# Performance work log

Measured on AMD Instinct MI355X. Metric: run time of the kernel, lower is better.

The kernel has to match this reference:

```python
import jax, jax.numpy as jnp
import numpy as np

T, HID, H = 1024, 2048, 16
LQ, LKV = 1536, 512
DR, DN, DQ, DV = 64, 128, 192, 128
HI, DI, TOPK = 16, 128, 256
EPS = 1e-6
NEG = -1e30


def _rms(x, g, eps=EPS):
    return x * jax.lax.rsqrt(jnp.mean(x * x, -1, keepdims=True) + eps) * g


def _ln(x, w, b, eps=1e-6):
    m = jnp.mean(x, -1, keepdims=True)
    v = jnp.mean((x - m) ** 2, -1, keepdims=True)
    return (x - m) * jax.lax.rsqrt(v + eps) * w + b


def _rope_interleave(x, cos, sin):
    # HF apply_rotary_pos_emb_interleave: de-interleave even/odd then standard rotate_half.
    x1, x2 = x[..., 0::2], x[..., 1::2]
    xr = jnp.concatenate([x1, x2], -1)
    rot = jnp.concatenate([-x2, x1], -1)
    return xr * cos + rot * sin


def _sparse_indices(hidden, q_lat, cos, sin, ks, ke, i_wqb, i_wk, i_ln_w, i_ln_b, i_wproj):
    # hidden [T,HID], q_lat [T,LQ]; returns [T,TOPK] int32 (sentinel index = T)
    t = hidden.shape[0]
    q_idx = (q_lat @ i_wqb.T).reshape(t, HI, DI)
    k_idx = _ln(hidden @ i_wk.T, i_ln_w, i_ln_b)          # [T,DI]
    w = hidden @ i_wproj.T                                 # [T,HI]
    q_pe = _rope_interleave(q_idx[..., :DR], cos[:, None, :], sin[:, None, :])
    k_pe = _rope_interleave(k_idx[..., :DR], cos, sin)
    qi = jnp.concatenate([q_pe, q_idx[..., DR:]], -1)      # [T,HI,DI]
    ki = jnp.concatenate([k_pe, k_idx[..., DR:]], -1)      # [T,DI]
    weight_scale = DI ** -0.5 * HI ** -0.5
    logits = jnp.einsum('thd,sd->ths', qi, ki)             # [T,HI,T]
    score = jnp.einsum('ths,th->ts', jax.nn.relu(logits), w) * weight_scale
    pos = jnp.arange(t)
    valid = (pos[None, :] >= ks[:, None]) & (pos[None, :] <= ke[:, None])
    score = jnp.where(valid, score, NEG)
    vals, idx = jax.lax.top_k(score, TOPK)
    return jnp.where(vals <= NEG / 2, t, idx).astype(jnp.int32)


def reference(hidden_states, cos, sin, ks, ke,
              w_qa, g_qa, w_qb, w_kva, g_kva, w_kvb, w_o,
              i_wqb, i_wk, i_ln_w, i_ln_b, i_wproj):
    t = hidden_states.shape[1]
    # low-rank projections
    q_lat = _rms(hidden_states @ w_qa.T, g_qa)             # [1,T,LQ]
    ckv = hidden_states @ w_kva.T                          # [1,T,LKV+DR]
    k_c = _rms(ckv[..., :LKV], g_kva)                      # [1,T,LKV]
    k_r = _rope_interleave(ckv[..., LKV:], cos[None], sin[None])  # [1,T,DR]
    # fp8 indexer (reference math in fp32), no-grad in original
    indices = _sparse_indices(hidden_states[0], q_lat[0], cos, sin, ks, ke,
                              i_wqb, i_wk, i_ln_w, i_ln_b, i_wproj)  # [T,TOPK]
    # MLA up-proj with weight absorption
    q_full = (q_lat @ w_qb.T).reshape(1, t, H, DQ)
    q_nope, q_rope = q_full[..., :DN], q_full[..., DN:]
    q_rope = _rope_interleave(q_rope, cos[None, :, None, :], sin[None, :, None, :])
    w_b = w_kvb.reshape(H, DN + DV, LKV)
    w_kn, w_v = w_b[:, :DN, :], w_b[:, DN:, :]
    q_abs = jnp.einsum('bshd,hdk->bshk', q_nope, w_kn)     # absorb k_nope up-proj
    sq = jnp.concatenate([q_abs, q_rope], -1)[0]           # [T,H,LKV+DR]
    skv = jnp.concatenate([k_c, k_r], -1)[0]               # [T,LKV+DR]
    skv = jnp.concatenate([skv, jnp.zeros((1, LKV + DR), skv.dtype)], 0)  # sentinel row
    # sparse attention over gathered top-k KV rows
    kv_g = skv[indices]                                    # [T,TOPK,LKV+DR]
    logits = jnp.einsum('thd,tjd->thj', sq, kv_g) * (DQ ** -0.5)
    logits = jnp.where(indices[:, None, :] == t, NEG, logits)
    p = jax.nn.softmax(logits, -1)
    out = jnp.einsum('thj,tjk->thk', p, kv_g[..., :LKV])   # values = compressed kv
    o = jnp.einsum('thk,hdk->thd', out, w_v)               # un-absorb v up-proj
    return o.reshape(1, t, H * DV) @ w_o.T


def setup_inputs() -> dict:
    key = jax.random.key(0)
    k = jax.random.split(key, 12)
    n = lambda kk, shape, s: jax.random.normal(kk, shape, jnp.float32) * s
    pos = jnp.arange(T, dtype=jnp.float32)
    inv = 1.0 / (10000.0 ** (jnp.arange(0, DR, 2, dtype=jnp.float32) / DR))
    ang = pos[:, None] * inv[None, :]
    cos = jnp.concatenate([jnp.cos(ang), jnp.cos(ang)], -1)
    sin = jnp.concatenate([jnp.sin(ang), jnp.sin(ang)], -1)
    return dict(
        hidden_states=n(k[0], (1, T, HID), 1.0),
        cos=cos, sin=sin,
        ks=jnp.zeros((T,), jnp.int32),
        ke=jnp.arange(T, dtype=jnp.int32),  # causal: keys s <= t valid
        w_qa=n(k[1], (LQ, HID), HID ** -0.5),
        g_qa=jnp.ones((LQ,), jnp.float32),
        w_qb=n(k[2], (H * DQ, LQ), LQ ** -0.5),
        w_kva=n(k[3], (LKV + DR, HID), HID ** -0.5),
        g_kva=jnp.ones((LKV,), jnp.float32),
        w_kvb=n(k[4], (H * (DN + DV), LKV), LKV ** -0.5),
        w_o=n(k[5], (HID, H * DV), (H * DV) ** -0.5),
        i_wqb=n(k[6], (HI * DI, LQ), LQ ** -0.5),
        i_wk=n(k[7], (DI, HID), HID ** -0.5),
        i_ln_w=jnp.ones((DI,), jnp.float32),
        i_ln_b=jnp.zeros((DI,), jnp.float32),
        i_wproj=n(k[8], (HI, HID), HID ** -0.5),
    )
```

## Files before the change

### kernel.cpp

```cpp
#include <hip/hip_runtime.h>
#include <hip/hip_bf16.h>
#include <cmath>

#define T_ 1024
#define HID_ 2048
#define H_ 16
#define LQ_ 1536
#define LKV_ 512
#define DR_ 64
#define DN_ 128
#define DQ_ 192
#define DV_ 128
#define HI_ 16
#define DI_ 128
#define TOPK_ 256
#define NEGF (-1e30f)

typedef short bfrag_t __attribute__((ext_vector_type(8)));
typedef float f32x4 __attribute__((ext_vector_type(4)));

__device__ __forceinline__ float wave_sum64(float v) {
#pragma unroll
  for (int off = 32; off; off >>= 1) v += __shfl_xor(v, off);
  return v;
}

#define GLL(g, l) __builtin_amdgcn_global_load_lds((const __attribute__((address_space(1))) void*)(g), \
                                     (__attribute__((address_space(3))) void*)(l), 16, 0, 0)

__global__ __launch_bounds__(256) void zero_k(float4* __restrict__ p, int n4) {
  int i = blockIdx.x * 256 + threadIdx.x;
  if (i < n4) p[i] = make_float4(0.f, 0.f, 0.f, 0.f);
}

template<typename CT>
__global__ __launch_bounds__(256) void gemm_bf_k(
    const short* __restrict__ A, int lda, long long sA,
    const short* __restrict__ B, int ldb, long long sB,
    CT* __restrict__ C, int ldc, long long sC,
    int Nout, int K)
{
  __shared__ short As[2][128 * 32];
  __shared__ short Bs[2][128 * 32];
  A += (long long)blockIdx.z * sA;
  B += (long long)blockIdx.z * sB;
  C += (long long)blockIdx.z * sC;
  const int tid = threadIdx.x;
  const int bm = blockIdx.y * 128, bn = blockIdx.x * 128;
  const int wave = tid >> 6, lane = tid & 63;
  const int wm = (wave >> 1) * 64, wn = (wave & 1) * 64;
  const int sr = tid >> 2;
  const int scol = (tid & 3) * 8;
  const int m0 = lane & 15, koff = (lane >> 4) * 8;
  f32x4 acc[4][4] = {};
  const short* ga = A + (long long)(bm + sr) * lda + scol;
  const short* gb = B + (long long)(bn + sr) * ldb + scol;
#define STAGE_BF(buf, off) \
    GLL(ga + (off), As[buf] + tid * 8); GLL(ga + (off) + 64 * lda, As[buf] + tid * 8 + 2048); \
    GLL(gb + (off), Bs[buf] + tid * 8); GLL(gb + (off) + 64 * ldb, Bs[buf] + tid * 8 + 2048);
  const int niter = K >> 5;
  STAGE_BF(0, 0);
  for (int it = 0; it < niter; ++it) {
    const int cur = it & 1;
    if (it + 1 < niter) {
      STAGE_BF(cur ^ 1, (it + 1) * 32);
      asm volatile("s_waitcnt vmcnt(4)\ns_barrier" ::: "memory");
    } else {
      asm volatile("s_waitcnt vmcnt(0)\ns_barrier" ::: "memory");
    }
    bfrag_t af[4], bfv[4];
#pragma unroll
    for (int i = 0; i < 4; ++i)
      af[i] = *(const bfrag_t*)(As[cur] + (wm + i * 16 + m0) * 32 + koff);
#pragma unroll
    for (int j = 0; j < 4; ++j)
      bfv[j] = *(const bfrag_t*)(Bs[cur] + (wn + j * 16 + m0) * 32 + koff);
#pragma unroll
    for (int i = 0; i < 4; ++i)
#pragma unroll
      for (int j = 0; j < 4; ++j)
        acc[i][j] = __builtin_amdgcn_mfma_f32_16x16x32_bf16(af[i], bfv[j], acc[i][j], 0, 0, 0);
    asm volatile("s_barrier" ::: "memory");
  }
#undef STAGE_BF
  const int cr = (lane >> 4) * 4, cc = lane & 15;
#pragma unroll
  for (int i = 0; i < 4; ++i) {
    int row = bm + wm + i * 16 + cr;
#pragma unroll
    for (int j = 0; j < 4; ++j) {
      int col = bn + wn + j * 16 + cc;
      if (col < Nout) {
#pragma unroll
        for (int r = 0; r < 4; ++r)
          C[(long long)(row + r) * ldc + col] = (CT)(acc[i][j][r]);
      }
    }
  }
}

__global__ __launch_bounds__(256) void gemm_bfs_k(
    const short* __restrict__ A, int lda,
    const short* __restrict__ B, int ldb,
    float* __restrict__ C, int ldc, int Nout, int K)
{
  __shared__ short As[2][128 * 32];
  __shared__ short Bs[2][128 * 32];
  const long long kbase = (long long)blockIdx.z * K;
  const int tid = threadIdx.x;
  const int bm = blockIdx.y * 128, bn = blockIdx.x * 128;
  const int wave = tid >> 6, lane = tid & 63;
  const int wm = (wave >> 1) * 64, wn = (wave & 1) * 64;
  const int sr = tid >> 2;
  const int scol = (tid & 3) * 8;
  const int m0 = lane & 15, koff = (lane >> 4) * 8;
  f32x4 acc[4][4] = {};
  const short* ga = A + (long long)(bm + sr) * lda + kbase + scol;
  const short* gb = B + (long long)(bn + sr) * ldb + kbase + scol;
#define STAGE_BS(buf, off) \
    GLL(ga + (off), As[buf] + tid * 8); GLL(ga + (off) + 64 * lda, As[buf] + tid * 8 + 2048); \
    GLL(gb + (off), Bs[buf] + tid * 8); GLL(gb + (off) + 64 * ldb, Bs[buf] + tid * 8 + 2048);
  const int niter = K >> 5;
  STAGE_BS(0, 0);
  for (int it = 0; it < niter; ++it) {
    const int cur = it & 1;
    if (it + 1 < niter) {
      STAGE_BS(cur ^ 1, (it + 1) * 32);
      asm volatile("s_waitcnt vmcnt(4)\ns_barrier" ::: "memory");
    } else {
      asm volatile("s_waitcnt vmcnt(0)\ns_barrier" ::: "memory");
    }
    bfrag_t af[4], bfv[4];
#pragma unroll
    for (int i = 0; i < 4; ++i)
      af[i] = *(const bfrag_t*)(As[cur] + (wm + i * 16 + m0) * 32 + koff);
#pragma unroll
    for (int j = 0; j < 4; ++j)
      bfv[j] = *(const bfrag_t*)(Bs[cur] + (wn + j * 16 + m0) * 32 + koff);
#pragma unroll
    for (int i = 0; i < 4; ++i)
#pragma unroll
      for (int j = 0; j < 4; ++j)
        acc[i][j] = __builtin_amdgcn_mfma_f32_16x16x32_bf16(af[i], bfv[j], acc[i][j], 0, 0, 0);
    asm volatile("s_barrier" ::: "memory");
  }
#undef STAGE_BS
  const int cr = (lane >> 4) * 4, cc = lane & 15;
#pragma unroll
  for (int i = 0; i < 4; ++i) {
    int row = bm + wm + i * 16 + cr;
#pragma unroll
    for (int j = 0; j < 4; ++j) {
      int col = bn + wn + j * 16 + cc;
      if (col < Nout) {
#pragma unroll
        for (int r = 0; r < 4; ++r)
          atomicAdd(&C[(long long)(row + r) * ldc + col], acc[i][j][r]);
      }
    }
  }
}

__global__ __launch_bounds__(256) void gemm3_k(
    const short* __restrict__ Ah, const short* __restrict__ Al, int lda,
    const short* __restrict__ Bh, const short* __restrict__ Bl, int ldb,
    float* __restrict__ C, int ldc, int Nout, int K)
{
  __shared__ short Ahs[2][128 * 32];
  __shared__ short Als[2][128 * 32];
  __shared__ short Bhs[2][128 * 32];
  __shared__ short Bls[2][128 * 32];
  const long long kbase = (long long)blockIdx.z * K;
  const int tid = threadIdx.x;
  const int bm = blockIdx.y * 128, bn = blockIdx.x * 128;
  const int wave = tid >> 6, lane = tid & 63;
  const int wm = (wave >> 1) * 64, wn = (wave & 1) * 64;
  const int sr = tid >> 2;
  const int scol = (tid & 3) * 8;
  const int m0 = lane & 15, koff = (lane >> 4) * 8;
  f32x4 acc[4][4] = {};
  const short* gah = Ah + (long long)(bm + sr) * lda + kbase + scol;
  const short* gal = Al + (long long)(bm + sr) * lda + kbase + scol;
  const short* gbh = Bh + (long long)(bn + sr) * ldb + kbase + scol;
  const short* gbl = Bl + (long long)(bn + sr) * ldb + kbase + scol;
#define STAGE_3(buf, off) \
    GLL(gah + (off), Ahs[buf] + tid * 8); GLL(gah + (off) + 64 * lda, Ahs[buf] + tid * 8 + 2048); \
    GLL(gal + (off), Als[buf] + tid * 8); GLL(gal + (off) + 64 * lda, Als[buf] + tid * 8 + 2048); \
    GLL(gbh + (off), Bhs[buf] + tid * 8); GLL(gbh + (off) + 64 * ldb, Bhs[buf] + tid * 8 + 2048); \
    GLL(gbl + (off), Bls[buf] + tid * 8); GLL(gbl + (off) + 64 * ldb, Bls[buf] + tid * 8 + 2048);
  const int niter = K >> 5;
  STAGE_3(0, 0);
  for (int it = 0; it < niter; ++it) {
    const int cur = it & 1;
    if (it + 1 < niter) {
      STAGE_3(cur ^ 1, (it + 1) * 32);
      asm volatile("s_waitcnt vmcnt(8)\ns_barrier" ::: "memory");
    } else {
      asm volatile("s_waitcnt vmcnt(0)\ns_barrier" ::: "memory");
    }
    bfrag_t afh[4], afl[4], bfh[4], bfl[4];
#pragma unroll
    for (int i = 0; i < 4; ++i) {
      afh[i] = *(const bfrag_t*)(Ahs[cur] + (wm + i * 16 + m0) * 32 + koff);
      afl[i] = *(const bfrag_t*)(Als[cur] + (wm + i * 16 + m0) * 32 + koff);
    }
#pragma unroll
    for (int j = 0; j < 4; ++j) {
      bfh[j] = *(const bfrag_t*)(Bhs[cur] + (wn + j * 16 + m0) * 32 + koff);
      bfl[j] = *(const bfrag_t*)(Bls[cur] + (wn + j * 16 + m0) * 32 + koff);
    }
#pragma unroll
    for (int i = 0; i < 4; ++i)
#pragma unroll
      for (int j = 0; j < 4; ++j)
        acc[i][j] = __builtin_amdgcn_mfma_f32_16x16x32_bf16(afh[i], bfh[j], acc[i][j], 0, 0, 0);
#pragma unroll
    for (int i = 0; i < 4; ++i)
#pragma unroll
      for (int j = 0; j < 4; ++j)
        acc[i][j] = __builtin_amdgcn_mfma_f32_16x16x32_bf16(afh[i], bfl[j], acc[i][j], 0, 0, 0);
#pragma unroll
    for (int i = 0; i < 4; ++i)
#pragma unroll
      for (int j = 0; j < 4; ++j)
        acc[i][j] = __builtin_amdgcn_mfma_f32_16x16x32_bf16(afl[i], bfh[j], acc[i][j], 0, 0, 0);
    asm volatile("s_barrier" ::: "memory");
  }
#undef STAGE_3
  const int cr = (lane >> 4) * 4, cc = lane & 15;
  const bool spl = (gridDim.z > 1);
#pragma unroll
  for (int i = 0; i < 4; ++i) {
    int row = bm + wm + i * 16 + cr;
#pragma unroll
    for (int j = 0; j < 4; ++j) {
      int col = bn + wn + j * 16 + cc;
      if (col < Nout) {
#pragma unroll
        for (int r = 0; r < 4; ++r) {
          if (spl) atomicAdd(&C[(long long)(row + r) * ldc + col], acc[i][j][r]);
          else     C[(long long)(row + r) * ldc + col] = acc[i][j][r];
        }
      }
    }
  }
}

__global__ __launch_bounds__(256) void score_gemm_k(
    const short* __restrict__ Ah, const short* __restrict__ Al,
    const short* __restrict__ Bh, const short* __restrict__ Bl,
    const float* __restrict__ wproj, const int* __restrict__ ks,
    const int* __restrict__ ke, float* __restrict__ scores)
{
  __shared__ short Ahs[2][128 * 32];
  __shared__ short Als[2][128 * 32];
  __shared__ short Bhs[2][128 * 32];
  __shared__ short Bls[2][128 * 32];
  __shared__ float s_w[8][16];
  __shared__ int s_ks[8], s_ke[8];
  const int tid = threadIdx.x;
  const int bm = blockIdx.y * 128, bn = blockIdx.x * 128;
  const int wave = tid >> 6, lane = tid & 63;
  const int wm = (wave >> 1) * 64, wn = (wave & 1) * 64;
  const int sr = tid >> 2;
  const int scol = (tid & 3) * 8;
  const int m0 = lane & 15, koff = (lane >> 4) * 8;
  const int t0 = bm >> 4;
  if (tid < 128) s_w[tid >> 4][tid & 15] =
      wproj[(t0 + (tid >> 4)) * HI_ + (tid & 15)] * 0.022097086912079608f;
  if (tid < 8) { s_ks[tid] = ks[t0 + tid]; s_ke[tid] = ke[t0 + tid]; }
  f32x4 acc[4][4] = {};
  const short* gah = Ah + (long long)(bm + sr) * DI_ + scol;
  const short* gal = Al + (long long)(bm + sr) * DI_ + scol;
  const short* gbh = Bh + (long long)(bn + sr) * DI_ + scol;
  const short* gbl = Bl + (long long)(bn + sr) * DI_ + scol;
#define STAGE_S(buf, off) \
    GLL(gah + (off), Ahs[buf] + tid * 8); GLL(gah + (off) + 64 * DI_, Ahs[buf] + tid * 8 + 2048); \
    GLL(gal + (off), Als[buf] + tid * 8); GLL(gal + (off) + 64 * DI_, Als[buf] + tid * 8 + 2048); \
    GLL(gbh + (off), Bhs[buf] + tid * 8); GLL(gbh + (off) + 64 * DI_, Bhs[buf] + tid * 8 + 2048); \
    GLL(gbl + (off), Bls[buf] + tid * 8); GLL(gbl + (off) + 64 * DI_, Bls[buf] + tid * 8 + 2048);
  const int niter = DI_ >> 5;
  STAGE_S(0, 0);
  for (int it = 0; it < niter; ++it) {
    const int cur = it & 1;
    if (it + 1 < niter) {
      STAGE_S(cur ^ 1, (it + 1) * 32);
      asm volatile("s_waitcnt vmcnt(8)\ns_barrier" ::: "memory");
    } else {
      asm volatile("s_waitcnt vmcnt(0)\ns_barrier" ::: "memory");
    }
    bfrag_t afh[4], afl[4], bfh[4], bfl[4];
#pragma unroll
    for (int i = 0; i < 4; ++i) {
      afh[i] = *(const bfrag_t*)(Ahs[cur] + (wm + i * 16 + m0) * 32 + koff);
      afl[i] = *(const bfrag_t*)(Als[cur] + (wm + i * 16 + m0) * 32 + koff);
    }
#pragma unroll
    for (int j = 0; j < 4; ++j) {
      bfh[j] = *(const bfrag_t*)(Bhs[cur] + (wn + j * 16 + m0) * 32 + koff);
      bfl[j] = *(const bfrag_t*)(Bls[cur] + (wn + j * 16 + m0) * 32 + koff);
    }
#pragma unroll
    for (int i = 0; i < 4; ++i)
#pragma unroll
      for (int j = 0; j < 4; ++j)
        acc[i][j] = __builtin_amdgcn_mfma_f32_16x16x32_bf16(afh[i], bfh[j], acc[i][j], 0, 0, 0);
#pragma unroll
    for (int i = 0; i < 4; ++i)
#pragma unroll
      for (int j = 0; j < 4; ++j)
        acc[i][j] = __builtin_amdgcn_mfma_f32_16x16x32_bf16(afh[i], bfl[j], acc[i][j], 0, 0, 0);
#pragma unroll
    for (int i = 0; i < 4; ++i)
#pragma unroll
      for (int j = 0; j < 4; ++j)
        acc[i][j] = __builtin_amdgcn_mfma_f32_16x16x32_bf16(afl[i], bfh[j], acc[i][j], 0, 0, 0);
    asm volatile("s_barrier" ::: "memory");
  }
#undef STAGE_S
  const int cc = lane & 15, quad = lane >> 4;
#pragma unroll
  for (int i = 0; i < 4; ++i) {
    const int g = (wm >> 4) + i;
    const int tok = t0 + g;
    const int lo = s_ks[g], hi = s_ke[g];
#pragma unroll
    for (int j = 0; j < 4; ++j) {
      float sc = 0.f;
#pragma unroll
      for (int r = 0; r < 4; ++r)
        sc += fmaxf(acc[i][j][r], 0.f) * s_w[g][quad * 4 + r];
      sc += __shfl_xor(sc, 16);
      sc += __shfl_xor(sc, 32);
      if (quad == 0) {
        const int s = bn + wn + j * 16 + cc;
        scores[tok * T_ + s] = (s >= lo && s <= hi) ? sc : NEGF;
      }
    }
  }
}

__global__ __launch_bounds__(256) void cast_bf16_k(const float* __restrict__ src,
                                                   __hip_bfloat16* __restrict__ dst, int n4) {
  int i = blockIdx.x * 256 + threadIdx.x;
  if (i >= n4) return;
  float4 v = ((const float4*)src)[i];
  union { ushort4 u; __hip_bfloat16 h[4]; } o;
  o.h[0] = __float2bfloat16(v.x); o.h[1] = __float2bfloat16(v.y);
  o.h[2] = __float2bfloat16(v.z); o.h[3] = __float2bfloat16(v.w);
  ((ushort4*)dst)[i] = o.u;
}

__global__ __launch_bounds__(256) void decomp_k(const float* __restrict__ src,
                                                __hip_bfloat16* __restrict__ hi,
                                                __hip_bfloat16* __restrict__ lo, int n4) {
  int i = blockIdx.x * 256 + threadIdx.x;
  if (i >= n4) return;
  float4 v = ((const float4*)src)[i];
  float f[4] = {v.x, v.y, v.z, v.w};
  union { ushort4 u; __hip_bfloat16 h[4]; } oh, ol;
#pragma unroll
  for (int j = 0; j < 4; ++j) {
    __hip_bfloat16 h = __float2bfloat16(f[j]);
    oh.h[j] = h;
    ol.h[j] = __float2bfloat16(f[j] - __bfloat162float(h));
  }
  ((ushort4*)hi)[i] = oh.u;
  ((ushort4*)lo)[i] = ol.u;
}

__global__ __launch_bounds__(256) void cast_pad_k(const float* __restrict__ src,
                                                  __hip_bfloat16* __restrict__ dst,
                                                  int N, int K4, int Npad) {
  int i = blockIdx.x * 256 + threadIdx.x;
  if (i >= Npad * K4) return;
  int r = i / K4;
  float4 v = make_float4(0.f, 0.f, 0.f, 0.f);
  if (r < N) v = ((const float4*)src)[i];
  union { ushort4 u; __hip_bfloat16 h[4]; } o;
  o.h[0] = __float2bfloat16(v.x); o.h[1] = __float2bfloat16(v.y);
  o.h[2] = __float2bfloat16(v.z); o.h[3] = __float2bfloat16(v.w);
  ((ushort4*)dst)[i] = o.u;
}

__global__ __launch_bounds__(256) void wkn_t_k(const float* __restrict__ wkvb,
                                               __hip_bfloat16* __restrict__ dst) {
  __shared__ float tile[64][65];
  const int h = blockIdx.z, k0 = blockIdx.y * 64, d0 = blockIdx.x * 64;
  const int c = threadIdx.x & 63, r0 = threadIdx.x >> 6;
#pragma unroll
  for (int rr = 0; rr < 16; ++rr) {
    int r = r0 + rr * 4;
    tile[r][c] = wkvb[((h * 256 + d0 + r) << 9) + k0 + c];
  }
  __syncthreads();
#pragma unroll
  for (int rr = 0; rr < 16; ++rr) {
    int r = r0 + rr * 4;
    dst[((h * 512 + k0 + r) << 7) + d0 + c] = __float2bfloat16(tile[c][r]);
  }
}

__global__ __launch_bounds__(256) void wv_cast_k(const float* __restrict__ wkvb,
                                                 __hip_bfloat16* __restrict__ dst) {
  int i = blockIdx.x * 256 + threadIdx.x;
  int k = i & 511, dv = (i >> 9) & 127, h = i >> 16;
  dst[i] = __float2bfloat16(wkvb[((h * 256 + 128 + dv) << 9) + k]);
}

__global__ __launch_bounds__(256) void rms_inplace_k(float* x, const float* __restrict__ g,
                                                     int C) {
  int t = blockIdx.x, tid = threadIdx.x;
  float* row = x + (long long)t * C;
  float ss = 0.f;
  for (int i = tid; i < C; i += 256) { float v = row[i]; ss += v * v; }
  __shared__ float red[4];
  ss = wave_sum64(ss);
  if ((tid & 63) == 0) red[tid >> 6] = ss;
  __syncthreads();
  float sc = rsqrtf((red[0] + red[1] + red[2] + red[3]) / (float)C + 1e-6f);
  for (int i = tid; i < C; i += 256) row[i] = row[i] * sc * g[i];
}

__global__ __launch_bounds__(256) void skv_build_k(const float* __restrict__ ckv,
                                                   const float* __restrict__ g,
                                                   const float* __restrict__ cosb,
                                                   const float* __restrict__ sinb,
                                                   __hip_bfloat16* __restrict__ skv) {
  int t = blockIdx.x, tid = threadIdx.x;
  __hip_bfloat16* out = skv + (long long)t * 576;
  if (t == T_) { for (int i = tid; i < 576; i += 256) out[i] = __float2bfloat16(0.f); return; }
  const float* row = ckv + (long long)t * 576;
  float ss = 0.f;
  for (int i = tid; i < 512; i += 256) { float v = row[i]; ss += v * v; }
  __shared__ float red[4];
  ss = wave_sum64(ss);
  if ((tid & 63) == 0) red[tid >> 6] = ss;
  __syncthreads();
  float sc = rsqrtf((red[0] + red[1] + red[2] + red[3]) / 512.f + 1e-6f);
  for (int i = tid; i < 512; i += 256) out[i] = __float2bfloat16(row[i] * sc * g[i]);
  if (tid < 64) {
    int j = tid, j2 = tid & 31;
    float c = cosb[t * 64 + j], s = sinb[t * 64 + j];
    float a = row[512 + 2 * j2], b = row[512 + 2 * j2 + 1];
    out[512 + j] = __float2bfloat16((j < 32) ? (a * c - b * s) : (a * s + b * c));
  }
}

__global__ __launch_bounds__(64) void rope_qi_k(float* qi, const float* __restrict__ cosb,
                                                const float* __restrict__ sinb) {
  int b = blockIdx.x, t = b >> 4, j = threadIdx.x, j2 = j & 31;
  float* x = qi + (long long)b * DI_;
  float c = cosb[t * 64 + j], s = sinb[t * 64 + j];
  float a = x[2 * j2], bb = x[2 * j2 + 1];
  float o = (j < 32) ? (a * c - bb * s) : (a * s + bb * c);
  x[j] = o;
}

__global__ __launch_bounds__(128) void ki_ln_rope_k(float* kbuf, const float* __restrict__ w,
                                                    const float* __restrict__ bia,
                                                    const float* __restrict__ cosb,
                                                    const float* __restrict__ sinb) {
  int t = blockIdx.x, i = threadIdx.x;
  float* row = kbuf + (long long)t * DI_;
  float x = row[i];
  __shared__ float red[2];
  float s1 = wave_sum64(x);
  if ((i & 63) == 0) red[i >> 6] = s1;
  __syncthreads();
  float mean = (red[0] + red[1]) / 128.f;
  float d = x - mean;
  __syncthreads();
  float s2 = wave_sum64(d * d);
  if ((i & 63) == 0) red[i >> 6] = s2;
  __syncthreads();
  float var = (red[0] + red[1]) / 128.f;
  float y = d * rsqrtf(var + 1e-6f) * w[i] + bia[i];
  __shared__ float rowl[128];
  rowl[i] = y;
  __syncthreads();
  float outv = y;
  if (i < 64) {
    int j2 = i & 31;
    float c = cosb[t * 64 + i], s = sinb[t * 64 + i];
    float a = rowl[2 * j2], b = rowl[2 * j2 + 1];
    outv = (i < 32) ? (a * c - b * s) : (a * s + b * c);
  }
  row[i] = outv;
}

__global__ __launch_bounds__(64) void rope_q_sq_k(const __hip_bfloat16* __restrict__ qfull,
                                                  const float* __restrict__ cosb,
                                                  const float* __restrict__ sinb,
                                                  __hip_bfloat16* __restrict__ sq) {
  int b = blockIdx.x, t = b >> 4, h = b & 15, j = threadIdx.x, j2 = j & 31;
  const __hip_bfloat16* x = qfull + (long long)t * 3072 + h * 192 + 128;
  float c = cosb[t * 64 + j], s = sinb[t * 64 + j];
  float a = __bfloat162float(x[2 * j2]), bb = __bfloat162float(x[2 * j2 + 1]);
  float o = (j < 32) ? (a * c - bb * s) : (a * s + bb * c);
  sq[((long long)t * H_ + h) * 576 + 512 + j] = __float2bfloat16(o);
}

__global__ __launch_bounds__(256) void wproj_k(const float* __restrict__ hidden,
                                               const float* __restrict__ wp,
                                               float* __restrict__ out) {
  int wave = threadIdx.x >> 6, lane = threadIdx.x & 63;
  int t = blockIdx.x * 4 + wave;
  const float4* x4 = (const float4*)(hidden + (long long)t * 2048);
  float acc[16] = {};
  for (int c = lane; c < 512; c += 64) {
    float4 xv = x4[c];
#pragma unroll
    for (int h = 0; h < 16; ++h) {
      float4 wv = ((const float4*)(wp + h * 2048))[c];
      acc[h] += xv.x * wv.x + xv.y * wv.y + xv.z * wv.z + xv.w * wv.w;
    }
  }
#pragma unroll
  for (int h = 0; h < 16; ++h) {
    float s = wave_sum64(acc[h]);
    if (lane == 0) out[t * 16 + h] = s;
  }
}

__global__ __launch_bounds__(256) void topk_k(const float* __restrict__ scores,
                                              int* __restrict__ indices)
{
  __shared__ unsigned s_hist[256];
  __shared__ unsigned s_wsum[4];
  __shared__ unsigned s_binsel[2];
  __shared__ unsigned s_cnt;
  const int t = blockIdx.x, tid = threadIdx.x;
  const int wave = tid >> 6, lane = tid & 63;
  const int i0 = tid * 4;
  if (tid == 0) s_cnt = 0;

  float4 sv = ((const float4*)(scores + t * T_))[tid];
  float f[4] = {sv.x, sv.y, sv.z, sv.w};
  unsigned key[4];
#pragma unroll
  for (int j = 0; j < 4; ++j) {
    unsigned u = __float_as_uint(f[j]);
    key[j] = (u & 0x80000000u) ? ~u : (u | 0x80000000u);
  }

  unsigned prefix = 0, Gprev = 0;
  for (int lvl = 0; lvl < 4; ++lvl) {
    const int shift = 24 - 8 * lvl;
    s_hist[tid] = 0;
    __syncthreads();
#pragma unroll
    for (int j = 0; j < 4; ++j) {
      unsigned k = key[j];
      bool part = (lvl == 0) || ((k >> (shift + 8)) == prefix);
      unsigned bin = (k >> shift) & 255u;
      unsigned long long mask = __ballot(part);
#pragma unroll
      for (int b = 0; b < 8; ++b) {
        unsigned long long bal = __ballot((bin >> b) & 1u);
        mask &= ((bin >> b) & 1u) ? bal : ~bal;
      }
      if (part && lane == (__ffsll((long long)mask) - 1))
        atomicAdd(&s_hist[bin], (unsigned)__popcll(mask));
    }
    __syncthreads();
    unsigned h = s_hist[255 - tid];
    unsigned sc_ = h;
    for (int off = 1; off < 64; off <<= 1) {
      unsigned v = __shfl_up(sc_, off);
      if (lane >= off) sc_ += v;
    }
    if (lane == 63) s_wsum[wave] = sc_;
    __syncthreads();
    unsigned wo = 0;
    for (int w = 0; w < wave; ++w) wo += s_wsum[w];
    unsigned incl = sc_ + wo, excl = incl - h;
    unsigned Rn = 256 - Gprev;
    if (excl < Rn && Rn <= incl) { s_binsel[0] = 255 - (unsigned)tid; s_binsel[1] = excl; }
    __syncthreads();
    prefix = (prefix << 8) | s_binsel[0];
    Gprev += s_binsel[1];
  }
  const unsigned thr = prefix;
  const unsigned Rq = 256 - Gprev;
  const unsigned negfkey = ~__float_as_uint(NEGF);

  unsigned eqc = 0;
#pragma unroll
  for (int j = 0; j < 4; ++j) eqc += (key[j] == thr) ? 1u : 0u;
  unsigned esc = eqc;
  for (int off = 1; off < 64; off <<= 1) {
    unsigned v = __shfl_up(esc, off);
    if (lane >= off) esc += v;
  }
  if (lane == 63) s_wsum[wave] = esc;
  __syncthreads();
  unsigned eo = 0;
  for (int w = 0; w < wave; ++w) eo += s_wsum[w];
  unsigned rank = esc + eo - eqc;

#pragma unroll
  for (int j = 0; j < 4; ++j) {
    unsigned k = key[j];
    int outv = (k == negfkey) ? T_ : (i0 + j);
    bool gt = (k > thr);
    unsigned long long bal = __ballot(gt);
    if (bal) {
      int leader = __ffsll((long long)bal) - 1;
      unsigned base = 0;
      if (lane == leader) base = atomicAdd(&s_cnt, (unsigned)__popcll(bal));
      base = (unsigned)__shfl((int)base, leader);
      if (gt) {
        unsigned pre = (unsigned)__popcll(bal & ((1ull << lane) - 1ull));
        indices[t * TOPK_ + base + pre] = outv;
      }
    }
    if (!gt && k == thr) {
      if (rank < Rq) indices[t * TOPK_ + Gprev + rank] = outv;
      rank++;
    }
  }
}

#define SP_LD 257
#define PB_LD 264
#define VT_LD 264
__global__ __launch_bounds__(512) void attn_k(
    const short* __restrict__ sq, const short* __restrict__ skv,
    const int* __restrict__ indices, __hip_bfloat16* __restrict__ attn_out)
{
  __shared__ int s_ind[TOPK_];
  __shared__ __align__(16) char s_un[2 * 64 * VT_LD * 2];
  float* s_p  = (float*)s_un;
  short* s_pb = (short*)(s_un + 16448);
  short* s_vt = (short*)s_un;
  const int t = blockIdx.x, tid = threadIdx.x;
  const int wave = tid >> 6, lane = tid & 63;
  const int m0 = lane & 15, quad = lane >> 4;
  if (tid < TOPK_) s_ind[tid] = indices[t * TOPK_ + tid];
  __syncthreads();

  {
    const int jb = wave * 32;
    int rows[2];
    const short* kvp[2];
#pragma unroll
    for (int j = 0; j < 2; ++j) {
      rows[j] = s_ind[jb + j * 16 + m0];
      kvp[j] = skv + rows[j] * 576 + quad * 8;
    }
    const short* qp = sq + ((long long)t * H_ + m0) * 576 + quad * 8;
    f32x4 qacc[2] = {};
    for (int ks = 0; ks < 18; ++ks) {
      const int k0 = ks * 32;
      bfrag_t aq = *(const bfrag_t*)(qp + k0);
#pragma unroll
      for (int j = 0; j < 2; ++j) {
        bfrag_t bq = *(const bfrag_t*)(kvp[j] + k0);
        qacc[j] = __builtin_amdgcn_mfma_f32_16x16x32_bf16(aq, bq, qacc[j], 0, 0, 0);
      }
    }
    const float scale = 0.07216878364870322f;
#pragma unroll
    for (int j = 0; j < 2; ++j) {
      int key = jb + j * 16 + m0;
      bool msk = (rows[j] == T_);
#pragma unroll
      for (int r = 0; r < 4; ++r)
        s_p[(quad * 4 + r) * SP_LD + key] = msk ? NEGF : qacc[j][r] * scale;
    }
  }
  __syncthreads();

  for (int h = wave * 2; h < wave * 2 + 2; ++h) {
    float* ph = s_p + h * SP_LD;
    float m = -3.4e38f;
    for (int j = lane; j < TOPK_; j += 64) m = fmaxf(m, ph[j]);
#pragma unroll
    for (int off = 32; off; off >>= 1) m = fmaxf(m, __shfl_xor(m, off));
    float sum = 0.f;
    for (int j = lane; j < TOPK_; j += 64) {
      float e = __expf(ph[j] - m);
      ph[j] = e; sum += e;
    }
    sum = wave_sum64(sum);
    float inv = 1.f / sum;
    for (int j = lane; j < TOPK_; j += 64) ph[j] *= inv;
  }
  __syncthreads();

  {
    const int col = tid & 255, h0 = tid >> 8;
#pragma unroll
    for (int h = 0; h < 8; ++h) {
      const int hh = h0 + h * 2;
      s_pb[hh * PB_LD + col] =
          (short)__bfloat16_as_ushort(__float2bfloat16(s_p[hh * SP_LD + col]));
    }
  }
  __syncthreads();

  bfrag_t apf[8];
#pragma unroll
  for (int kk = 0; kk < 8; ++kk)
    apf[kk] = *(const bfrag_t*)(s_pb + m0 * PB_LD + kk * 32 + quad * 8);

  const int grp = wave >> 2, gw = wave & 3;
  short* svt = s_vt + grp * (64 * VT_LD);
  const int r8 = (tid >> 3) & 31;
  const int bb = tid & 7;

  for (int cc = 0; cc < 4; ++cc) {
    const int c = grp * 4 + cc;
    __syncthreads();
#pragma unroll
    for (int rep = 0; rep < 8; ++rep) {
      const int kv = r8 + 32 * rep;
      const int row = s_ind[kv];
      bfrag_t v = *(const bfrag_t*)(skv + (long long)row * 576 + c * 64 + bb * 8);
      const int colx = kv ^ (bb << 3);
#pragma unroll
      for (int j = 0; j < 8; ++j)
        svt[(bb * 8 + j) * VT_LD + colx] = v[j];
    }
    __syncthreads();
    const int d = gw * 16 + m0;
    const short* vrow = svt + d * VT_LD;
    const int sx = (d >> 3) << 3;
    f32x4 oacc = {0.f, 0.f, 0.f, 0.f};
#pragma unroll
    for (int kk = 0; kk < 8; ++kk) {
      bfrag_t bv = *(const bfrag_t*)(vrow + ((kk * 32 + quad * 8) ^ sx));
      oacc = __builtin_amdgcn_mfma_f32_16x16x32_bf16(apf[kk], bv, oacc, 0, 0, 0);
    }
    const int col = c * 64 + d;
#pragma unroll
    for (int r = 0; r < 4; ++r)
      attn_out[((long long)t * H_ + quad * 4 + r) * 512 + col] = __float2bfloat16(oacc[r]);
  }
}

extern "C" void kernel_launch(void* const* d_in, const int* in_sizes, int n_in,
                              void* d_out, int out_size, void* d_ws, size_t ws_size,
                              hipStream_t stream) {
  const float* hidden  = (const float*)d_in[0];
  const float* cosb    = (const float*)d_in[1];
  const float* sinb    = (const float*)d_in[2];
  const int*   ks      = (const int*)d_in[3];
  const int*   ke      = (const int*)d_in[4];
  const float* w_qa    = (const float*)d_in[5];
  const float* g_qa    = (const float*)d_in[6];
  const float* w_qb    = (const float*)d_in[7];
  const float* w_kva   = (const float*)d_in[8];
  const float* g_kva   = (const float*)d_in[9];
  const float* w_kvb   = (const float*)d_in[10];
  const float* w_o     = (const float*)d_in[11];
  const float* i_wqb   = (const float*)d_in[12];
  const float* i_wk    = (const float*)d_in[13];
  const float* i_ln_w  = (const float*)d_in[14];
  const float* i_ln_b  = (const float*)d_in[15];
  const float* i_wproj = (const float*)d_in[16];
  float* out = (float*)d_out;
  (void)in_sizes; (void)n_in; (void)out_size; (void)ws_size;

  char* ws = (char*)d_ws;
  __hip_bfloat16* hid_hi  = (__hip_bfloat16*)(ws + 0);
  __hip_bfloat16* hid_lo  = (__hip_bfloat16*)(ws + 4194304);
  float*          q_lat   = (float*)(ws + 8388608);
  __hip_bfloat16* qi_hi   = (__hip_bfloat16*)(ws + 8388608);
  __hip_bfloat16* qlat_hi = (__hip_bfloat16*)(ws + 14680064);
  __hip_bfloat16* qlat_lo = (__hip_bfloat16*)(ws + 17825792);
  float*          qi      = (float*)(ws + 20971520);
  float*          scoresb = (float*)(ws + 20971520);
  float*          kib     = (float*)(ws + 29360128);
  float*          wbuf    = (float*)(ws + 29884416);
  float*          ckv     = (float*)(ws + 29949952);
  __hip_bfloat16* qi_lo   = (__hip_bfloat16*)(ws + 29949952);
  __hip_bfloat16* ki_hi   = (__hip_bfloat16*)(ws + 34144256);
  __hip_bfloat16* ki_lo   = (__hip_bfloat16*)(ws + 34406400);
  __hip_bfloat16* sq_bf   = (__hip_bfloat16*)(ws + 0);
  __hip_bfloat16* o_bf    = (__hip_bfloat16*)(ws + 0);
  __hip_bfloat16* W       = (__hip_bfloat16*)(ws + 37748736);
  __hip_bfloat16* skv_bf  = (__hip_bfloat16*)(ws + 47185920);
  int*            idxb    = (int*)(ws + 48366720);
  __hip_bfloat16* E       = (__hip_bfloat16*)(ws + 49415296);

  dim3 blk(256);
  const short* Ws = (const short*)W;
  const short* Es = (const short*)E;

  decomp_k<<<2048, blk, 0, stream>>>(hidden, hid_hi, hid_lo, 524288);

  decomp_k<<<3072, blk, 0, stream>>>(w_qa, W, E, 786432);
  zero_k<<<1536, blk, 0, stream>>>((float4*)q_lat, 393216);
  gemm3_k<<<dim3(12, 8, 4), blk, 0, stream>>>(
      (const short*)hid_hi, (const short*)hid_lo, HID_, Ws, Es, HID_, q_lat, LQ_, LQ_, 512);
  rms_inplace_k<<<T_, blk, 0, stream>>>(q_lat, g_qa, LQ_);

  cast_pad_k<<<1280, blk, 0, stream>>>(w_kva, W, 576, 512, 640);
  zero_k<<<576, blk, 0, stream>>>((float4*)ckv, 147456);
  gemm_bfs_k<<<dim3(5, 8, 4), blk, 0, stream>>>(
      (const short*)hid_hi, HID_, Ws, HID_, ckv, 576, 576, 512);
  skv_build_k<<<T_ + 1, blk, 0, stream>>>(ckv, g_kva, cosb, sinb, skv_bf);

  decomp_k<<<1536, blk, 0, stream>>>(q_lat, qlat_hi, qlat_lo, 393216);

  decomp_k<<<3072, blk, 0, stream>>>(i_wqb, W, E, 786432);
  zero_k<<<2048, blk, 0, stream>>>((float4*)qi, 524288);
  gemm3_k<<<dim3(16, 8, 4), blk, 0, stream>>>(
      (const short*)qlat_hi, (const short*)qlat_lo, LQ_, Ws, Es, LQ_, qi, HI_ * DI_, HI_ * DI_, 384);
  rope_qi_k<<<T_ * HI_, dim3(64), 0, stream>>>(qi, cosb, sinb);
  decomp_k<<<2048, blk, 0, stream>>>(qi, qi_hi, qi_lo, 524288);

  decomp_k<<<256, blk, 0, stream>>>(i_wk, W, E, 65536);
  zero_k<<<128, blk, 0, stream>>>((float4*)kib, 32768);
  gemm3_k<<<dim3(1, 8, 16), blk, 0, stream>>>(
      (const short*)hid_hi, (const short*)hid_lo, HID_, Ws, Es, HID_, kib, DI_, DI_, 128);
  ki_ln_rope_k<<<T_, dim3(128), 0, stream>>>(kib, i_ln_w, i_ln_b, cosb, sinb);
  decomp_k<<<128, blk, 0, stream>>>(kib, ki_hi, ki_lo, 32768);

  wproj_k<<<256, blk, 0, stream>>>(hidden, i_wproj, wbuf);

  score_gemm_k<<<dim3(8, 128), blk, 0, stream>>>(
      (const short*)qi_hi, (const short*)qi_lo, (const short*)ki_hi, (const short*)ki_lo,
      wbuf, ks, ke, scoresb);
  topk_k<<<T_, blk, 0, stream>>>(scoresb, idxb);

  cast_bf16_k<<<4608, blk, 0, stream>>>(w_qb, W, 1179648);
  gemm_bf_k<__hip_bfloat16><<<dim3(24, 8, 1), blk, 0, stream>>>(
      (const short*)qlat_hi, LQ_, 0, Ws, LQ_, 0, (__hip_bfloat16*)E, H_ * DQ_, 0, H_ * DQ_, LQ_);
  rope_q_sq_k<<<T_ * H_, dim3(64), 0, stream>>>(E, cosb, sinb, sq_bf);

  wkn_t_k<<<dim3(2, 8, 16), blk, 0, stream>>>(w_kvb, W);
  gemm_bf_k<__hip_bfloat16><<<dim3(4, 8, 16), blk, 0, stream>>>(
      Es, H_ * DQ_, 192, Ws, DI_, 65536, sq_bf, H_ * 576, 576, LKV_, DN_);

  attn_k<<<T_, dim3(512), 0, stream>>>((const short*)sq_bf, (const short*)skv_bf, idxb, E);

  wv_cast_k<<<4096, blk, 0, stream>>>(w_kvb, W);
  gemm_bf_k<__hip_bfloat16><<<dim3(1, 8, 16), blk, 0, stream>>>(
      Es, H_ * LKV_, 512, Ws, LKV_, 65536, o_bf, H_ * DV_, 128, DV_, LKV_);

  cast_bf16_k<<<4096, blk, 0, stream>>>(w_o, W, 1048576);
  zero_k<<<2048, blk, 0, stream>>>((float4*)out, 524288);
  gemm_bfs_k<<<dim3(16, 8, 4), blk, 0, stream>>>(
      (const short*)o_bf, H_ * DV_, Ws, H_ * DV_, out, HID_, HID_, 512);
}
```

Baseline: 542.6 us.

## Stage Q and gathered KV rows through LDS with double-buffered async loads in attention

The sparse attention kernel now loads the per-token query block into shared memory once. The gathered KV rows are streamed through a double-buffered LDS tile using global-to-LDS async loads, with waitcnt and barriers so that the next k-step load overlaps the current MFMA step. This is meant to replace scattered per-lane global loads with coalesced row loads and hide their latency. The cost is about 76 KB of LDS per block, which lowers occupancy, plus two barriers per k-step.

```diff
diff --git a/kernel.cpp b/kernel.cpp
--- a/kernel.cpp
+++ b/kernel.cpp
@@ -630,10 +630,12 @@
     const int* __restrict__ indices, __hip_bfloat16* __restrict__ attn_out)
 {
   __shared__ int s_ind[TOPK_];
-  __shared__ __align__(16) char s_un[2 * 64 * VT_LD * 2];
-  float* s_p  = (float*)s_un;
-  short* s_pb = (short*)(s_un + 16448);
+  __shared__ __align__(16) char s_un[76096];
+  short* s_q  = (short*)s_un;
+  short* s_k  = (short*)(s_un + 18432);
+  float* s_p  = (float*)(s_un + 51200);
   short* s_vt = (short*)s_un;
+  short* s_pb = (short*)(s_un + 67648);
   const int t = blockIdx.x, tid = threadIdx.x;
   const int wave = tid >> 6, lane = tid & 63;
   const int m0 = lane & 15, quad = lane >> 4;
@@ -641,30 +643,53 @@
   __syncthreads();
 
   {
+#pragma unroll
+    for (int n = 0; n < 2; ++n) {
+      const int c = n * 512 + tid;
+      const int qks = c >> 6, qrow = (c >> 2) & 15, qch = c & 3;
+      GLL(sq + ((long long)t * H_ + qrow) * 576 + qks * 32 + qch * 8, s_q + c * 8);
+    }
+    if (tid < 128) {
+      const int c = 1024 + tid;
+      const int qks = c >> 6, qrow = (c >> 2) & 15, qch = c & 3;
+      GLL(sq + ((long long)t * H_ + qrow) * 576 + qks * 32 + qch * 8, s_q + c * 8);
+    }
+  }
+
+  {
     const int jb = wave * 32;
-    int rows[2];
-    const short* kvp[2];
-#pragma unroll
-    for (int j = 0; j < 2; ++j) {
-      rows[j] = s_ind[jb + j * 16 + m0];
-      kvp[j] = skv + rows[j] * 576 + quad * 8;
-    }
-    const short* qp = sq + ((long long)t * H_ + m0) * 576 + quad * 8;
+    const int rA = s_ind[jb + (lane >> 2)];
+    const int rB = s_ind[jb + 16 + (lane >> 2)];
+    const short* pA = skv + (long long)rA * 576 + (lane & 3) * 8;
+    const short* pB = skv + (long long)rB * 576 + (lane & 3) * 8;
+    short* ldsA = s_k + wave * 1024 + lane * 8;
+#define STAGE_K(buf, kstep) \
+    GLL(pA + (kstep) * 32, ldsA + (buf) * 8192); \
+    GLL(pB + (kstep) * 32, ldsA + (buf) * 8192 + 512);
     f32x4 qacc[2] = {};
+    STAGE_K(0, 0);
     for (int ks = 0; ks < 18; ++ks) {
-      const int k0 = ks * 32;
-      bfrag_t aq = *(const bfrag_t*)(qp + k0);
+      const int cur = ks & 1;
+      if (ks + 1 < 18) {
+        STAGE_K(cur ^ 1, ks + 1);
+        asm volatile("s_waitcnt vmcnt(2)\ns_barrier" ::: "memory");
+      } else {
+        asm volatile("s_waitcnt vmcnt(0)\ns_barrier" ::: "memory");
+      }
+      bfrag_t aq = *(const bfrag_t*)(s_q + ks * 512 + m0 * 32 + quad * 8);
 #pragma unroll
       for (int j = 0; j < 2; ++j) {
-        bfrag_t bq = *(const bfrag_t*)(kvp[j] + k0);
+        bfrag_t bq = *(const bfrag_t*)(s_k + cur * 8192 + (jb + j * 16 + m0) * 32 + quad * 8);
         qacc[j] = __builtin_amdgcn_mfma_f32_16x16x32_bf16(aq, bq, qacc[j], 0, 0, 0);
       }
-    }
+      asm volatile("s_barrier" ::: "memory");
+    }
+#undef STAGE_K
     const float scale = 0.07216878364870322f;
 #pragma unroll
     for (int j = 0; j < 2; ++j) {
       int key = jb + j * 16 + m0;
-      bool msk = (rows[j] == T_);
+      bool msk = (s_ind[key] == T_);
 #pragma unroll
       for (int r = 0; r < 4; ++r)
         s_p[(quad * 4 + r) * SP_LD + key] = msk ? NEGF : qacc[j][r] * scale;
```

Result: faster. 531.3 us (-2.1%).
